# Performance work log

Measured on AMD Instinct MI355X. Metric: run time of the kernel, lower is better.

## Reference

```python
import jax, jax.numpy as jnp
import numpy as np

N = 8192
IN_F = 512
OUT_F = 512
N_SUB = 8


def setup_inputs() -> dict:
    key = jax.random.key(0)
    k1, k2, k3, k4 = jax.random.split(key, 4)
    input_features = jax.random.normal(k1, (N, IN_F), dtype=jnp.float32)
    # dense adjacency with small positive entries (normalized-adj-like)
    adj = jax.random.uniform(k2, (N, N), dtype=jnp.float32) / N
    subspace_labels = jax.random.randint(k3, (N,), 0, N_SUB, dtype=jnp.int32)
    # kaiming-uniform-style init per subspace weight
    bound = float(np.sqrt(6.0 / IN_F))
    W = jax.random.uniform(k4, (N_SUB, IN_F, OUT_F), dtype=jnp.float32,
                           minval=-bound, maxval=bound)
    return {"input_features": input_features, "adj": adj,
            "subspace_labels": subspace_labels, "W": W}


def reference(input_features, adj, subspace_labels, W):
    # Original: for each subspace s,
    #   output[mask_s] = adj[mask_s][:, mask_s] @ (X[mask_s] @ W[s])
    # Equivalently: per-node support uses that node's subspace weight, and
    # adjacency is masked to same-subspace pairs.
    n_sub = W.shape[0]
    support = jnp.zeros((input_features.shape[0], W.shape[2]),
                        dtype=input_features.dtype)
    for s in range(n_sub):  # small fixed loop over subspaces
        sel = (subspace_labels == s)[:, None]
        support = support + jnp.where(sel, input_features @ W[s], 0.0)
    # mask adjacency to intra-subspace edges: [N, N]
    same = (subspace_labels[:, None] == subspace_labels[None, :])
    masked_adj = jnp.where(same, adj, 0.0)
    return masked_adj @ support
```

## Files before the change

### kernel.cpp

```cpp
#include <hip/hip_runtime.h>
#include <hip/hip_bf16.h>

#define NN   8192
#define FF   512
#define NS   8
#define CAP  1152
#define KKT  (NS * CAP)

typedef __bf16 bf16x8 __attribute__((ext_vector_type(8)));
typedef float  f32x4  __attribute__((ext_vector_type(4)));

__global__ __launch_bounds__(256) void prep_kernel(
        const float* __restrict__ W, __bf16* __restrict__ WT,
        const int* __restrict__ labels, int* __restrict__ permP,
        int* __restrict__ kk_of) {
    if (blockIdx.x < 2048) {
        __shared__ float tile[32][33];
        const int id = blockIdx.x;
        const int n0 = (id & 15) * 32, k0 = ((id >> 4) & 15) * 32, s = id >> 8;
        const int t = threadIdx.x, tx = t & 31, ty = t >> 5;
        const float* Ws = W + (size_t)s * FF * FF;
        #pragma unroll
        for (int r = 0; r < 4; ++r)
            tile[ty + r * 8][tx] = Ws[(size_t)(k0 + ty + r * 8) * FF + n0 + tx];
        __syncthreads();
        __bf16* WTs = WT + (size_t)s * FF * FF;
        #pragma unroll
        for (int r = 0; r < 4; ++r)
            WTs[(size_t)(n0 + ty + r * 8) * FF + k0 + tx] = (__bf16)tile[tx][ty + r * 8];
    } else {
        __shared__ int off8[NS];
        const int t = threadIdx.x, lane = t & 63;
        if (t < NS) off8[t] = 0;
        for (int i = t; i < KKT; i += 256) permP[i] = -1;
        __syncthreads();
        for (int i = t; i < NN; i += 256) {
            int s = labels[i];
            int pos = -1;
            #pragma unroll
            for (int ss = 0; ss < NS; ++ss) {
                unsigned long long mask = __ballot(s == ss);
                if (s == ss) {
                    int leader = __ffsll((unsigned long long)mask) - 1;
                    int nbelow = __popcll(mask & ((1ull << lane) - 1ull));
                    int base = 0;
                    if (lane == leader) base = atomicAdd(&off8[ss], __popcll(mask));
                    base = __shfl(base, leader);
                    pos = base + nbelow;
                }
            }
            if (pos >= 0 && pos < CAP) {
                int kk = s * CAP + pos;
                permP[kk] = i;
                kk_of[i] = kk;
            } else {
                kk_of[i] = -1;
            }
        }
    }
}

__global__ __launch_bounds__(256) void support_kernel(
        const float* __restrict__ X, const __bf16* __restrict__ WT,
        const int* __restrict__ permP, __bf16* __restrict__ supT) {
    __shared__ __align__(16) __bf16 Alds[4][33][8];
    __shared__ __align__(16) __bf16 Blds[4][257][8];
    __shared__ int nodes[32];
    const int t = threadIdx.x, lane = t & 63, w = t >> 6;
    const int ii0 = blockIdx.x * 32;
    const int ncol0 = blockIdx.y * 256;
    const int seg = ii0 / CAP;
    const int mh = w & 1, nq = w >> 1, l15 = lane & 15, q = lane >> 4;
    f32x4 acc[8] = {};
    if (t < 32) nodes[t] = permP[ii0 + t];
    __syncthreads();
    const __bf16* Wseg = WT + (size_t)seg * FF * FF;
    const int am = t >> 3, ac = t & 7;
    for (int k0 = 0; k0 < FF; k0 += 32) {
        #pragma unroll
        for (int pass = 0; pass < 4; ++pass) {
            int slot = pass * 256 + t;
            int cc = slot & 3, n = slot >> 2;
            *(uint4*)&Blds[cc][n][0] =
                *(const uint4*)(Wseg + (size_t)(ncol0 + n) * FF + k0 + cc * 8);
        }
        {
            int node = nodes[am];
            __align__(8) __bf16 v[4];
            if (node >= 0) {
                float4 xv = *(const float4*)(X + (size_t)node * FF + k0 + ac * 4);
                v[0] = (__bf16)xv.x; v[1] = (__bf16)xv.y;
                v[2] = (__bf16)xv.z; v[3] = (__bf16)xv.w;
            } else {
                v[0] = v[1] = v[2] = v[3] = (__bf16)0.0f;
            }
            *(uint2*)&Alds[ac >> 1][am][(ac & 1) * 4] = *(uint2*)v;
        }
        __syncthreads();
        bf16x8 af = *(bf16x8*)&Alds[q][mh * 16 + l15][0];
        int nbase = nq * 128 + l15;
        #pragma unroll
        for (int nt = 0; nt < 8; ++nt) {
            bf16x8 bfr = *(bf16x8*)&Blds[q][nbase + nt * 16][0];
            acc[nt] = __builtin_amdgcn_mfma_f32_16x16x32_bf16(af, bfr, acc[nt], 0, 0, 0);
        }
        __syncthreads();
    }
    int kkb = ii0 + mh * 16 + q * 4;
    #pragma unroll
    for (int nt = 0; nt < 8; ++nt) {
        int n = ncol0 + nq * 128 + nt * 16 + l15;
        __align__(8) __bf16 v[4];
        #pragma unroll
        for (int r = 0; r < 4; ++r) v[r] = (__bf16)acc[nt][r];
        *(uint2*)(supT + (size_t)n * KKT + kkb) = *(uint2*)v;
    }
}

__global__ __launch_bounds__(256) void compact_kernel(
        const float* __restrict__ adj, const int* __restrict__ permP,
        const int* __restrict__ kk_of, __bf16* __restrict__ adjc) {
    __shared__ __align__(16) __bf16 rows[4][CAP];
    const int t = threadIdx.x;
    const int ii0 = blockIdx.x * 4;
    const int base = (ii0 / CAP) * CAP;
    for (int j = t; j < 4 * CAP / 2; j += 256) ((unsigned int*)rows)[j] = 0u;
    int nodes[4];
    #pragma unroll
    for (int r = 0; r < 4; ++r) nodes[r] = permP[ii0 + r];
    __syncthreads();
    const int4* kkrow = (const int4*)kk_of;
    #pragma unroll
    for (int p = 0; p < NN / (256 * 4); ++p) {
        int idx = p * 256 + t;
        int4 kk = kkrow[idx];
        kk.x -= base; kk.y -= base; kk.z -= base; kk.w -= base;
        #pragma unroll
        for (int r = 0; r < 4; ++r) {
            int node = nodes[r];
            if (node < 0) continue;
            float4 a = *(const float4*)(adj + (size_t)node * NN + (size_t)idx * 4);
            if ((unsigned)kk.x < CAP) rows[r][kk.x] = (__bf16)a.x;
            if ((unsigned)kk.y < CAP) rows[r][kk.y] = (__bf16)a.y;
            if ((unsigned)kk.z < CAP) rows[r][kk.z] = (__bf16)a.z;
            if ((unsigned)kk.w < CAP) rows[r][kk.w] = (__bf16)a.w;
        }
    }
    __syncthreads();
    const uint4* src = (const uint4*)rows;
    uint4* dst = (uint4*)(adjc + (size_t)ii0 * CAP);
    for (int j = t; j < 4 * CAP * 2 / 16; j += 256) dst[j] = src[j];
}

__global__ __launch_bounds__(256) void gemm_kernel(
        const __bf16* __restrict__ adjc, const __bf16* __restrict__ supT,
        const int* __restrict__ permP, float* __restrict__ out) {
    __shared__ __align__(16) __bf16 Alds[4][33][8];
    __shared__ __align__(16) __bf16 Blds[4][257][8];
    const int t = threadIdx.x, lane = t & 63, w = t >> 6;
    const int ii0 = blockIdx.x * 32;
    const int ncol0 = blockIdx.y * 256;
    const int seg = ii0 / CAP, base = seg * CAP;
    const int mh = w & 1, nq = w >> 1, l15 = lane & 15, q = lane >> 4;
    f32x4 acc[8] = {};
    const __bf16* Ag = adjc + (size_t)ii0 * CAP;
    for (int j0 = 0; j0 < CAP; j0 += 32) {
        #pragma unroll
        for (int pass = 0; pass < 4; ++pass) {
            int slot = pass * 256 + t;
            int cc = slot & 3, n = slot >> 2;
            *(uint4*)&Blds[cc][n][0] =
                *(const uint4*)(supT + (size_t)(ncol0 + n) * KKT + base + j0 + cc * 8);
        }
        if (t < 128) {
            int m = t >> 2, cc = t & 3;
            *(uint4*)&Alds[cc][m][0] =
                *(const uint4*)(Ag + (size_t)m * CAP + j0 + cc * 8);
        }
        __syncthreads();
        bf16x8 af = *(bf16x8*)&Alds[q][mh * 16 + l15][0];
        int nbase = nq * 128 + l15;
        #pragma unroll
        for (int nt = 0; nt < 8; ++nt) {
            bf16x8 bfr = *(bf16x8*)&Blds[q][nbase + nt * 16][0];
            acc[nt] = __builtin_amdgcn_mfma_f32_16x16x32_bf16(af, bfr, acc[nt], 0, 0, 0);
        }
        __syncthreads();
    }
    int rowb = ii0 + mh * 16 + q * 4;
    #pragma unroll
    for (int r = 0; r < 4; ++r) {
        int node = permP[rowb + r];
        if (node >= 0) {
            float* o = out + (size_t)node * FF + ncol0 + nq * 128 + l15;
            #pragma unroll
            for (int nt = 0; nt < 8; ++nt) o[nt * 16] = acc[nt][r];
        }
    }
}

extern "C" void kernel_launch(void* const* d_in, const int* in_sizes, int n_in,
                              void* d_out, int out_size, void* d_ws, size_t ws_size,
                              hipStream_t stream) {
    const float* X      = (const float*)d_in[0];
    const float* adj    = (const float*)d_in[1];
    const int*   labels = (const int*)d_in[2];
    const float* W      = (const float*)d_in[3];
    float* out = (float*)d_out;

    char* ws = (char*)d_ws;
    int*    kk_of = (int*)(ws + 1024);
    int*    permP = (int*)(ws + (64u << 10));
    __bf16* WT    = (__bf16*)(ws + (1u << 20));
    __bf16* supT  = (__bf16*)(ws + (6u << 20));
    __bf16* adjc  = (__bf16*)(ws + (16u << 20));

    prep_kernel<<<2049, 256, 0, stream>>>(W, WT, labels, permP, kk_of);
    support_kernel<<<dim3(KKT / 32, 2), 256, 0, stream>>>(X, WT, permP, supT);
    compact_kernel<<<KKT / 4, 256, 0, stream>>>(adj, permP, kk_of, adjc);
    gemm_kernel<<<dim3(KKT / 32, 2), 256, 0, stream>>>(adjc, supT, permP, out);
}
```

Measured before the change: 529.9 us.

## Fuse support GEMM and adjacency compaction into one launch; widen tiles to full width

```diff
diff --git a/kernel.cpp b/kernel.cpp
--- a/kernel.cpp
+++ b/kernel.cpp
@@ -60,106 +60,114 @@
     }
 }
 
-__global__ __launch_bounds__(256) void support_kernel(
+union SmemU {
+    struct {
+        __bf16 A[4][32][8];
+        __bf16 B[4][512][8];
+        int    nodes[32];
+    } sup;
+    struct {
+        __bf16 rows[4][CAP];
+    } cmp;
+};
+
+__global__ __launch_bounds__(512) void mid_kernel(
         const float* __restrict__ X, const __bf16* __restrict__ WT,
-        const int* __restrict__ permP, __bf16* __restrict__ supT) {
-    __shared__ __align__(16) __bf16 Alds[4][33][8];
-    __shared__ __align__(16) __bf16 Blds[4][257][8];
-    __shared__ int nodes[32];
+        const float* __restrict__ adj, const int* __restrict__ permP,
+        const int* __restrict__ kk_of, __bf16* __restrict__ supT,
+        __bf16* __restrict__ adjc) {
+    __shared__ __align__(16) SmemU sm;
+    const int t = threadIdx.x;
+    const int sgrp = blockIdx.x / 9, r9 = blockIdx.x % 9;
+
+    if (r9 == 8) {
+        const int lane = t & 63, w = t >> 6;
+        const int ii0 = sgrp * 32;
+        const int seg = ii0 / CAP;
+        const int mh = w & 1, nq = w >> 1, l15 = lane & 15, q = lane >> 4;
+        f32x4 acc[8] = {};
+        if (t < 32) sm.sup.nodes[t] = permP[ii0 + t];
+        __syncthreads();
+        const __bf16* Wseg = WT + (size_t)seg * FF * FF;
+        for (int k0 = 0; k0 < FF; k0 += 32) {
+            #pragma unroll
+            for (int pass = 0; pass < 4; ++pass) {
+                int slot = pass * 512 + t;
+                int cc = slot & 3, n = slot >> 2;
+                *(uint4*)&sm.sup.B[cc][n][0] =
+                    *(const uint4*)(Wseg + (size_t)n * FF + k0 + cc * 8);
+            }
+            if (t < 256) {
+                int m = t >> 3, c = t & 7;
+                int node = sm.sup.nodes[m];
+                __align__(8) __bf16 v[4];
+                if (node >= 0) {
+                    float4 xv = *(const float4*)(X + (size_t)node * FF + k0 + c * 4);
+                    v[0] = (__bf16)xv.x; v[1] = (__bf16)xv.y;
+                    v[2] = (__bf16)xv.z; v[3] = (__bf16)xv.w;
+                } else {
+                    v[0] = v[1] = v[2] = v[3] = (__bf16)0.0f;
+                }
+                *(uint2*)&sm.sup.A[c >> 1][m][(c & 1) * 4] = *(uint2*)v;
+            }
+            __syncthreads();
+            bf16x8 af = *(bf16x8*)&sm.sup.A[q][mh * 16 + l15][0];
+            int nbase = nq * 128 + l15;
+            #pragma unroll
+            for (int nt = 0; nt < 8; ++nt) {
+                bf16x8 bfr = *(bf16x8*)&sm.sup.B[q][nbase + nt * 16][0];
+                acc[nt] = __builtin_amdgcn_mfma_f32_16x16x32_bf16(af, bfr, acc[nt], 0, 0, 0);
+            }
+            __syncthreads();
+        }
+        int kkb = ii0 + mh * 16 + q * 4;
+        #pragma unroll
+        for (int nt = 0; nt < 8; ++nt) {
+            int n = nq * 128 + nt * 16 + l15;
+            __align__(8) __bf16 v[4];
+            #pragma unroll
+            for (int rr = 0; rr < 4; ++rr) v[rr] = (__bf16)acc[nt][rr];
+            *(uint2*)(supT + (size_t)n * KKT + kkb) = *(uint2*)v;
+        }
+    } else {
+        const int ii0 = (sgrp * 8 + r9) * 4;
+        const int base = (ii0 / CAP) * CAP;
+        for (int j = t; j < 4 * CAP / 2; j += 512) ((unsigned int*)sm.cmp.rows)[j] = 0u;
+        int nodes[4];
+        #pragma unroll
+        for (int rr = 0; rr < 4; ++rr) nodes[rr] = permP[ii0 + rr];
+        __syncthreads();
+        const int4* kkrow = (const int4*)kk_of;
+        #pragma unroll
+        for (int p = 0; p < NN / (512 * 4); ++p) {
+            int idx = p * 512 + t;
+            int4 kk = kkrow[idx];
+            kk.x -= base; kk.y -= base; kk.z -= base; kk.w -= base;
+            #pragma unroll
+            for (int rr = 0; rr < 4; ++rr) {
+                int node = nodes[rr];
+                if (node < 0) continue;
+                float4 a = *(const float4*)(adj + (size_t)node * NN + (size_t)idx * 4);
+                if ((unsigned)kk.x < CAP) sm.cmp.rows[rr][kk.x] = (__bf16)a.x;
+                if ((unsigned)kk.y < CAP) sm.cmp.rows[rr][kk.y] = (__bf16)a.y;
+                if ((unsigned)kk.z < CAP) sm.cmp.rows[rr][kk.z] = (__bf16)a.z;
+                if ((unsigned)kk.w < CAP) sm.cmp.rows[rr][kk.w] = (__bf16)a.w;
+            }
+        }
+        __syncthreads();
+        const uint4* src = (const uint4*)sm.cmp.rows;
+        uint4* dst = (uint4*)(adjc + (size_t)ii0 * CAP);
+        for (int j = t; j < 4 * CAP * 2 / 16; j += 512) dst[j] = src[j];
+    }
+}
+
+__global__ __launch_bounds__(512) void gemm_kernel(
+        const __bf16* __restrict__ adjc, const __bf16* __restrict__ supT,
+        const int* __restrict__ permP, float* __restrict__ out) {
+    __shared__ __align__(16) __bf16 Alds[4][32][8];
+    __shared__ __align__(16) __bf16 Blds[4][512][8];
     const int t = threadIdx.x, lane = t & 63, w = t >> 6;
     const int ii0 = blockIdx.x * 32;
-    const int ncol0 = blockIdx.y * 256;
-    const int seg = ii0 / CAP;
-    const int mh = w & 1, nq = w >> 1, l15 = lane & 15, q = lane >> 4;
-    f32x4 acc[8] = {};
-    if (t < 32) nodes[t] = permP[ii0 + t];
-    __syncthreads();
-    const __bf16* Wseg = WT + (size_t)seg * FF * FF;
-    const int am = t >> 3, ac = t & 7;
-    for (int k0 = 0; k0 < FF; k0 += 32) {
-        #pragma unroll
-        for (int pass = 0; pass < 4; ++pass) {
-            int slot = pass * 256 + t;
-            int cc = slot & 3, n = slot >> 2;
-            *(uint4*)&Blds[cc][n][0] =
-                *(const uint4*)(Wseg + (size_t)(ncol0 + n) * FF + k0 + cc * 8);
-        }
-        {
-            int node = nodes[am];
-            __align__(8) __bf16 v[4];
-            if (node >= 0) {
-                float4 xv = *(const float4*)(X + (size_t)node * FF + k0 + ac * 4);
-                v[0] = (__bf16)xv.x; v[1] = (__bf16)xv.y;
-                v[2] = (__bf16)xv.z; v[3] = (__bf16)xv.w;
-            } else {
-                v[0] = v[1] = v[2] = v[3] = (__bf16)0.0f;
-            }
-            *(uint2*)&Alds[ac >> 1][am][(ac & 1) * 4] = *(uint2*)v;
-        }
-        __syncthreads();
-        bf16x8 af = *(bf16x8*)&Alds[q][mh * 16 + l15][0];
-        int nbase = nq * 128 + l15;
-        #pragma unroll
-        for (int nt = 0; nt < 8; ++nt) {
-            bf16x8 bfr = *(bf16x8*)&Blds[q][nbase + nt * 16][0];
-            acc[nt] = __builtin_amdgcn_mfma_f32_16x16x32_bf16(af, bfr, acc[nt], 0, 0, 0);
-        }
-        __syncthreads();
-    }
-    int kkb = ii0 + mh * 16 + q * 4;
-    #pragma unroll
-    for (int nt = 0; nt < 8; ++nt) {
-        int n = ncol0 + nq * 128 + nt * 16 + l15;
-        __align__(8) __bf16 v[4];
-        #pragma unroll
-        for (int r = 0; r < 4; ++r) v[r] = (__bf16)acc[nt][r];
-        *(uint2*)(supT + (size_t)n * KKT + kkb) = *(uint2*)v;
-    }
-}
-
-__global__ __launch_bounds__(256) void compact_kernel(
-        const float* __restrict__ adj, const int* __restrict__ permP,
-        const int* __restrict__ kk_of, __bf16* __restrict__ adjc) {
-    __shared__ __align__(16) __bf16 rows[4][CAP];
-    const int t = threadIdx.x;
-    const int ii0 = blockIdx.x * 4;
-    const int base = (ii0 / CAP) * CAP;
-    for (int j = t; j < 4 * CAP / 2; j += 256) ((unsigned int*)rows)[j] = 0u;
-    int nodes[4];
-    #pragma unroll
-    for (int r = 0; r < 4; ++r) nodes[r] = permP[ii0 + r];
-    __syncthreads();
-    const int4* kkrow = (const int4*)kk_of;
-    #pragma unroll
-    for (int p = 0; p < NN / (256 * 4); ++p) {
-        int idx = p * 256 + t;
-        int4 kk = kkrow[idx];
-        kk.x -= base; kk.y -= base; kk.z -= base; kk.w -= base;
-        #pragma unroll
-        for (int r = 0; r < 4; ++r) {
-            int node = nodes[r];
-            if (node < 0) continue;
-            float4 a = *(const float4*)(adj + (size_t)node * NN + (size_t)idx * 4);
-            if ((unsigned)kk.x < CAP) rows[r][kk.x] = (__bf16)a.x;
-            if ((unsigned)kk.y < CAP) rows[r][kk.y] = (__bf16)a.y;
-            if ((unsigned)kk.z < CAP) rows[r][kk.z] = (__bf16)a.z;
-            if ((unsigned)kk.w < CAP) rows[r][kk.w] = (__bf16)a.w;
-        }
-    }
-    __syncthreads();
-    const uint4* src = (const uint4*)rows;
-    uint4* dst = (uint4*)(adjc + (size_t)ii0 * CAP);
-    for (int j = t; j < 4 * CAP * 2 / 16; j += 256) dst[j] = src[j];
-}
-
-__global__ __launch_bounds__(256) void gemm_kernel(
-        const __bf16* __restrict__ adjc, const __bf16* __restrict__ supT,
-        const int* __restrict__ permP, float* __restrict__ out) {
-    __shared__ __align__(16) __bf16 Alds[4][33][8];
-    __shared__ __align__(16) __bf16 Blds[4][257][8];
-    const int t = threadIdx.x, lane = t & 63, w = t >> 6;
-    const int ii0 = blockIdx.x * 32;
-    const int ncol0 = blockIdx.y * 256;
     const int seg = ii0 / CAP, base = seg * CAP;
     const int mh = w & 1, nq = w >> 1, l15 = lane & 15, q = lane >> 4;
     f32x4 acc[8] = {};
@@ -167,10 +175,10 @@
     for (int j0 = 0; j0 < CAP; j0 += 32) {
         #pragma unroll
         for (int pass = 0; pass < 4; ++pass) {
-            int slot = pass * 256 + t;
+            int slot = pass * 512 + t;
             int cc = slot & 3, n = slot >> 2;
             *(uint4*)&Blds[cc][n][0] =
-                *(const uint4*)(supT + (size_t)(ncol0 + n) * KKT + base + j0 + cc * 8);
+                *(const uint4*)(supT + (size_t)n * KKT + base + j0 + cc * 8);
         }
         if (t < 128) {
             int m = t >> 2, cc = t & 3;
@@ -192,7 +200,7 @@
     for (int r = 0; r < 4; ++r) {
         int node = permP[rowb + r];
         if (node >= 0) {
-            float* o = out + (size_t)node * FF + ncol0 + nq * 128 + l15;
+            float* o = out + (size_t)node * FF + nq * 128 + l15;
             #pragma unroll
             for (int nt = 0; nt < 8; ++nt) o[nt * 16] = acc[nt][r];
         }
@@ -216,7 +224,6 @@
     __bf16* adjc  = (__bf16*)(ws + (16u << 20));
 
     prep_kernel<<<2049, 256, 0, stream>>>(W, WT, labels, permP, kk_of);
-    support_kernel<<<dim3(KKT / 32, 2), 256, 0, stream>>>(X, WT, permP, supT);
-    compact_kernel<<<KKT / 4, 256, 0, stream>>>(adj, permP, kk_of, adjc);
-    gemm_kernel<<<dim3(KKT / 32, 2), 256, 0, stream>>>(adjc, supT, permP, out);
-}
+    mid_kernel<<<2592, 512, 0, stream>>>(X, WT, adj, permP, kk_of, supT, adjc);
+    gemm_kernel<<<KKT / 32, 512, 0, stream>>>(adjc, supT, permP, out);
+}
```

New measurement: 515.9 us. 2.6% less time.
